# Optimization experiments

Measured on AMD Instinct MI355X. Metric: run time of the kernel, lower is better.

Reference implementation:

```python
import jax, jax.numpy as jnp
import numpy as np

N = 50000          # nodes
E = 800000         # directed edges (before self loops)
H = 2              # attention heads
NEG_SLOPE = 0.2    # PyG GATv2 default
EPS = 1e-5         # GraphNorm eps
DIMS = [(3, 64), (64, 64), (64, 64)]


def _gatv2_layer(x, Wl, Wr, att, b, src, dst):
    # x: [N, din]; Wl, Wr: [din, H*C]; att: [H, C]; b: [C]
    n = x.shape[0]
    h, c = att.shape
    xl = (x @ Wl).reshape(n, h, c)   # source-side transform
    xr = (x @ Wr).reshape(n, h, c)   # target-side transform
    # edge-wise GATv2 score: a . leaky_relu(xl[j] + xr[i])
    e = jax.nn.leaky_relu(xl[src] + xr[dst], NEG_SLOPE)      # [E, H, C]
    logit = jnp.einsum('ehc,hc->eh', e, att)                 # [E, H]
    # segment softmax over incoming edges of each target node
    m = jax.ops.segment_max(logit, dst, num_segments=n)      # [N, H]
    a = jnp.exp(logit - m[dst])
    z = jax.ops.segment_sum(a, dst, num_segments=n)
    alpha = a / z[dst]                                       # [E, H]
    out = jax.ops.segment_sum(alpha[:, :, None] * xl[src], dst, num_segments=n)  # [N, H, C]
    return out.mean(axis=1) + b                              # concat=False -> head mean


def _graph_norm(x, w, b, ms):
    # single-graph GraphNorm: x -> w * (x - ms*mean) / sqrt(var + eps) + b
    mu = x.mean(axis=0)
    o = x - ms * mu
    var = (o * o).mean(axis=0)
    return w * o * jax.lax.rsqrt(var + EPS) + b


def setup_inputs() -> dict:
    key = jax.random.key(0)
    ks = jax.random.split(key, 2 + 3 * len(DIMS))
    inp = {
        'x': jax.random.normal(ks[0], (N, 3), dtype=jnp.float32),
        'edge_index': jax.random.randint(ks[1], (2, E), 0, N, dtype=jnp.int32),
    }
    for i, (din, dout) in enumerate(DIMS, start=1):
        k0, k1, k2 = ks[2 + 3 * (i - 1):2 + 3 * i]
        s_in = np.float32(1.0 / np.sqrt(din))
        s_att = np.float32(1.0 / np.sqrt(dout))
        inp[f'Wl{i}'] = jax.random.normal(k0, (din, H * dout), dtype=jnp.float32) * s_in
        inp[f'Wr{i}'] = jax.random.normal(k1, (din, H * dout), dtype=jnp.float32) * s_in
        inp[f'att{i}'] = jax.random.normal(k2, (H, dout), dtype=jnp.float32) * s_att
        inp[f'b{i}'] = jnp.zeros((dout,), dtype=jnp.float32)
        inp[f'gw{i}'] = jnp.ones((dout,), dtype=jnp.float32)
        inp[f'gb{i}'] = jnp.zeros((dout,), dtype=jnp.float32)
        inp[f'gm{i}'] = jnp.ones((dout,), dtype=jnp.float32)
    return inp


def reference(x, edge_index,
              Wl1, Wr1, att1, b1, gw1, gb1, gm1,
              Wl2, Wr2, att2, b2, gw2, gb2, gm2,
              Wl3, Wr3, att3, b3, gw3, gb3, gm3):
    n = x.shape[0]
    loop = jnp.arange(n, dtype=edge_index.dtype)
    src = jnp.concatenate([edge_index[0], loop])  # add_self_loops=True
    dst = jnp.concatenate([edge_index[1], loop])
    layers = [(Wl1, Wr1, att1, b1, gw1, gb1, gm1),
              (Wl2, Wr2, att2, b2, gw2, gb2, gm2),
              (Wl3, Wr3, att3, b3, gw3, gb3, gm3)]
    for Wl, Wr, att, b, gw, gb, gm in layers:
        x = _gatv2_layer(x, Wl, Wr, att, b, src, dst)
        x = jax.nn.relu(_graph_norm(x, gw, gb, gm))
    return x
```

## Files before the change

### kernel.cpp

```cpp
#include <hip/hip_runtime.h>
#include <math.h>

#define NN 50000
#define NE 800000
#define TE (NE + NN)
#define HC 128
#define NEG_SLOPE 0.2f
#define EPSV 1e-5f
#define NBUCK 64
#define GGRID 782
#define WTB 128
#define ZB 52
#define ZERO_N4 18644

typedef __attribute__((ext_vector_type(8))) short bf16x8;
typedef __attribute__((ext_vector_type(4))) float f32x4;
union BfU { uint4 u; bf16x8 b; };

__device__ __forceinline__ unsigned short f2bf(float x) {
    unsigned u = __float_as_uint(x);
    unsigned r = (u + 0x7fff + ((u >> 16) & 1)) >> 16;
    return (unsigned short)r;
}


__global__ __launch_bounds__(256) void count_k(const int* __restrict__ dst,
                                               int* __restrict__ cnt,
                                               int* __restrict__ rank) {
    int e = blockIdx.x * 256 + threadIdx.x;
    if (e >= TE) return;
    int d = (e < NE) ? dst[e] : (e - NE);
    rank[e] = atomicAdd(&cnt[d], 1);
}

__global__ __launch_bounds__(1024) void scan1_k(const int* __restrict__ cnt,
                                                int* __restrict__ excl,
                                                int* __restrict__ aux) {
    __shared__ int wsum[16];
    int tid = threadIdx.x;
    int gid = blockIdx.x * 1024 + tid;
    int lane = tid & 63, wid = tid >> 6;
    int v = (gid < NN) ? cnt[gid] : 0;
    int x = v;
#pragma unroll
    for (int off = 1; off < 64; off <<= 1) {
        int t = __shfl_up(x, off, 64);
        if (lane >= off) x += t;
    }
    if (lane == 63) wsum[wid] = x;
    __syncthreads();
    if (wid == 0 && lane < 16) {
        int y = wsum[lane];
#pragma unroll
        for (int off = 1; off < 16; off <<= 1) {
            int t = __shfl_up(y, off, 64);
            if (lane >= off) y += t;
        }
        wsum[lane] = y;
    }
    __syncthreads();
    int base = (wid > 0) ? wsum[wid - 1] : 0;
    int incl = base + x;
    if (gid < NN) excl[gid] = incl - v;
    if (tid == 1023) aux[blockIdx.x] = incl;
}

__global__ __launch_bounds__(256) void scatter_k(const int* __restrict__ srcp,
                                                 const int* __restrict__ dstp,
                                                 const int* __restrict__ excl,
                                                 const int* __restrict__ aux,
                                                 const int* __restrict__ rank,
                                                 int* __restrict__ row_ptr,
                                                 int* __restrict__ col,
                                                 int nblk) {
    __shared__ int auxs[64];
    if (threadIdx.x < 64) {
        int lane = threadIdx.x;
        int v = (lane < nblk) ? aux[lane] : 0;
        int x = v;
#pragma unroll
        for (int off = 1; off < 64; off <<= 1) {
            int t = __shfl_up(x, off, 64);
            if (lane >= off) x += t;
        }
        auxs[lane] = x - v;
    }
    __syncthreads();
    int e = blockIdx.x * 256 + threadIdx.x;
    if (e >= TE) return;
    if (e <= NN) row_ptr[e] = (e == NN) ? TE : excl[e] + auxs[e >> 10];
    int s, d;
    if (e < NE) { s = srcp[e]; d = dstp[e]; } else { s = e - NE; d = s; }
    col[excl[d] + auxs[d >> 10] + rank[e]] = s << 8;
}

__device__ __forceinline__ void store_xlp(char* xlp, int row, int c0, const float* a) {
    unsigned hsel = (unsigned)c0 >> 6;
    unsigned dd = (unsigned)c0 & 31;
    unsigned sub = (c0 & 32) ? 2u : 0u;
    char* q = xlp + (size_t)row * 256 + hsel * 128 + 4 * dd + sub;
#pragma unroll
    for (int j = 0; j < 4; ++j)
        *(unsigned short*)(q + 4 * j) = f2bf(a[j]);
}


__global__ __launch_bounds__(256) void init_k(const float* __restrict__ x,
                                              const float* __restrict__ Wl1,
                                              const float* __restrict__ Wr1,
                                              char* __restrict__ xlp,
                                              float* __restrict__ xr,
                                              const float* __restrict__ Wl2,
                                              const float* __restrict__ Wr2,
                                              const float* __restrict__ Wl3,
                                              const float* __restrict__ Wr3,
                                              unsigned short* __restrict__ wt2,
                                              unsigned short* __restrict__ wt3,
                                              float4* __restrict__ zero4) {
    __shared__ float xs[32][72];
    __shared__ float ws[32][260];
    int b = blockIdx.x;
    int tid = threadIdx.x;

    if (b >= GGRID) {
        if (b < GGRID + WTB) {
            int idx = (b - GGRID) * 256 + tid;
            int l = idx >> 14;
            int rem = idx & 16383;
            int k = rem >> 8;
            int c = rem & 255;
            const float* W = (l == 0) ? (c < 128 ? Wl2 : Wr2) : (c < 128 ? Wl3 : Wr3);
            float v = W[k * 128 + (c & 127)];
            unsigned short* wt = (l == 0) ? wt2 : wt3;
            wt[c * 64 + k] = f2bf(v);
        } else {
            float4 zv; zv.x = zv.y = zv.z = zv.w = 0.f;
            for (int i = (b - GGRID - WTB) * 256 + tid; i < ZERO_N4; i += ZB * 256)
                zero4[i] = zv;
        }
        return;
    }

    int row0 = b * 64;
    int row_t = (tid >> 5) * 8;
    int c0 = (tid & 31) * 4;
    const int K = 3;

    float acc0[8][4];
    float acc1[8][4];
#pragma unroll
    for (int i = 0; i < 8; ++i)
#pragma unroll
        for (int j = 0; j < 4; ++j) { acc0[i][j] = 0.f; acc1[i][j] = 0.f; }

    for (int i = tid; i < 64 * K; i += 256) {
        int r = i / K;
        int k = i - r * K;
        int row = row0 + r;
        xs[k][r] = (row < NN) ? x[(size_t)row * K + k] : 0.f;
    }
    for (int i = tid; i < K * 64; i += 256) {
        int k = i >> 6;
        int cq = i & 63;
        const float* srcp = (cq < 32) ? &Wl1[(size_t)k * 128 + cq * 4]
                                      : &Wr1[(size_t)k * 128 + (cq - 32) * 4];
        float4 v = *(const float4*)srcp;
        *(float4*)&ws[k][cq * 4] = v;
    }
    __syncthreads();
    for (int k = 0; k < K; ++k) {
        float4 a0 = *(float4*)&xs[k][row_t];
        float4 a1 = *(float4*)&xs[k][row_t + 4];
        float4 b0 = *(float4*)&ws[k][c0];
        float4 b1 = *(float4*)&ws[k][c0 + 128];
        float av[8] = {a0.x, a0.y, a0.z, a0.w, a1.x, a1.y, a1.z, a1.w};
        float bl[4] = {b0.x, b0.y, b0.z, b0.w};
        float br[4] = {b1.x, b1.y, b1.z, b1.w};
#pragma unroll
        for (int i = 0; i < 8; ++i)
#pragma unroll
            for (int j = 0; j < 4; ++j) {
                acc0[i][j] += av[i] * bl[j];
                acc1[i][j] += av[i] * br[j];
            }
    }
#pragma unroll
    for (int i = 0; i < 8; ++i) {
        int row = row0 + row_t + i;
        if (row < NN) {
            store_xlp(xlp, row, c0, acc0[i]);
            float4 o1; o1.x = acc1[i][0]; o1.y = acc1[i][1]; o1.z = acc1[i][2]; o1.w = acc1[i][3];
            *(float4*)&xr[(size_t)row * HC + c0] = o1;
        }
    }
}

__device__ __forceinline__ void reduce_stats(const float* __restrict__ stats,
                                             const float* __restrict__ gw,
                                             const float* __restrict__ gb,
                                             const float* __restrict__ gm,
                                             float (*part)[128],
                                             float* __restrict__ cf_out) {
    int tid = threadIdx.x;
    int w = tid >> 6;
    int lane = tid & 63;
    float s = 0.f, s2 = 0.f;
    for (int b = 16 * w; b < 16 * w + 16; ++b) {
        s += stats[b * 128 + lane];
        s2 += stats[b * 128 + 64 + lane];
    }
    part[w][lane] = s;
    part[w][64 + lane] = s2;
    __syncthreads();
    if (tid < 64) {
        int c = tid;
        float sum = (part[0][c] + part[1][c]) + (part[2][c] + part[3][c]);
        float sum2 = (part[0][64 + c] + part[1][64 + c]) + (part[2][64 + c] + part[3][64 + c]);
        float inv_n = 1.f / (float)NN;
        float mu = sum * inv_n;
        float ex2 = sum2 * inv_n;
        float g = gm[c];
        float var = ex2 - 2.f * g * mu * mu + g * g * mu * mu;
        float rs = rsqrtf(var + EPSV);
        cf_out[c] = gw[c] * rs;
        cf_out[64 + c] = gb[c] - gw[c] * rs * g * mu;
    }
    __syncthreads();
}


__global__ __launch_bounds__(256) void gemm_mfma(const unsigned* __restrict__ hbf,
                                                 const float* __restrict__ stats,
                                                 const float* __restrict__ gw,
                                                 const float* __restrict__ gb,
                                                 const float* __restrict__ gm,
                                                 const unsigned short* __restrict__ wt,
                                                 char* __restrict__ xlp,
                                                 float* __restrict__ xr,
                                                 int n) {
    __shared__ unsigned short xs[64][72];
    __shared__ float part[4][128];
    __shared__ float cfS[128];
    int tid = threadIdx.x;
    int row0 = blockIdx.x * 64;

    reduce_stats(stats, gw, gb, gm, part, cfS);

    {
        int r = tid >> 2;
        int q = tid & 3;
        int row = row0 + r;
        unsigned pk[8];
        if (row < n) {
            const unsigned* hp = hbf + (size_t)row * 32 + (q & 1) * 16;
            uint4 u0 = *(const uint4*)(hp + 0);
            uint4 u1 = *(const uint4*)(hp + 4);
            uint4 u2 = *(const uint4*)(hp + 8);
            uint4 u3 = *(const uint4*)(hp + 12);
            unsigned hv[16] = {u0.x, u0.y, u0.z, u0.w, u1.x, u1.y, u1.z, u1.w,
                               u2.x, u2.y, u2.z, u2.w, u3.x, u3.y, u3.z, u3.w};
            bool hi = (q >> 1) != 0;
#pragma unroll
            for (int i = 0; i < 4; ++i) {
                float4 v;
                v.x = hi ? __uint_as_float(hv[4 * i + 0] & 0xffff0000u) : __uint_as_float(hv[4 * i + 0] << 16);
                v.y = hi ? __uint_as_float(hv[4 * i + 1] & 0xffff0000u) : __uint_as_float(hv[4 * i + 1] << 16);
                v.z = hi ? __uint_as_float(hv[4 * i + 2] & 0xffff0000u) : __uint_as_float(hv[4 * i + 2] << 16);
                v.w = hi ? __uint_as_float(hv[4 * i + 3] & 0xffff0000u) : __uint_as_float(hv[4 * i + 3] << 16);
                float4 cw = *(const float4*)&cfS[q * 16 + 4 * i];
                float4 cb = *(const float4*)&cfS[64 + q * 16 + 4 * i];
                float r0 = fmaxf(fmaf(cw.x, v.x, cb.x), 0.f);
                float r1 = fmaxf(fmaf(cw.y, v.y, cb.y), 0.f);
                float r2 = fmaxf(fmaf(cw.z, v.z, cb.z), 0.f);
                float r3 = fmaxf(fmaf(cw.w, v.w, cb.w), 0.f);
                pk[2 * i]     = (unsigned)f2bf(r0) | ((unsigned)f2bf(r1) << 16);
                pk[2 * i + 1] = (unsigned)f2bf(r2) | ((unsigned)f2bf(r3) << 16);
            }
        } else {
#pragma unroll
            for (int i = 0; i < 8; ++i) pk[i] = 0;
        }
        uint4* dst = (uint4*)&xs[r][q * 16];
        dst[0] = make_uint4(pk[0], pk[1], pk[2], pk[3]);
        dst[1] = make_uint4(pk[4], pk[5], pk[6], pk[7]);
    }
    __syncthreads();

    int w = tid >> 6;
    int lane = tid & 63;
    int m = lane & 15;
    int quad = lane >> 4;

    BfU a0, a1;
    a0.u = *(const uint4*)&xs[16 * w + m][quad * 8];
    a1.u = *(const uint4*)&xs[16 * w + m][32 + quad * 8];

    const char* wtb = (const char*)wt + (size_t)(m * 128 + quad * 16);

    f32x4 acc[16];
#pragma unroll
    for (int c = 0; c < 16; ++c) acc[c] = (f32x4){0.f, 0.f, 0.f, 0.f};
#pragma unroll
    for (int c = 0; c < 16; ++c) {
        BfU b0, b1;
        b0.u = *(const uint4*)(wtb + c * 2048);
        b1.u = *(const uint4*)(wtb + c * 2048 + 64);
        acc[c] = __builtin_amdgcn_mfma_f32_16x16x32_bf16(a0.b, b0.b, acc[c], 0, 0, 0);
        acc[c] = __builtin_amdgcn_mfma_f32_16x16x32_bf16(a1.b, b1.b, acc[c], 0, 0, 0);
    }

    int rbase = row0 + 16 * w + quad * 4;
#pragma unroll
    for (int c = 8; c < 16; ++c) {
        int colx = 16 * (c - 8) + m;
#pragma unroll
        for (int r = 0; r < 4; ++r) {
            int row = rbase + r;
            if (row < n) xr[(size_t)row * 128 + colx] = acc[c][r];
        }
    }
#pragma unroll
    for (int pi = 0; pi < 4; ++pi) {
        int c = (pi & 1) + (pi >> 1) * 4;
        int head = pi >> 1;
        int dd = (pi & 1) * 16 + m;
#pragma unroll
        for (int r = 0; r < 4; ++r) {
            int row = rbase + r;
            if (row < n) {
                unsigned val = (unsigned)f2bf(acc[c][r]) | ((unsigned)f2bf(acc[c + 2][r]) << 16);
                *(unsigned*)(xlp + (size_t)row * 256 + head * 128 + 4 * dd) = val;
            }
        }
    }
}


__global__ __launch_bounds__(256) void coef_k(const float* __restrict__ stats,
                                              const float* __restrict__ gw,
                                              const float* __restrict__ gb,
                                              const float* __restrict__ gm,
                                              float* __restrict__ cf) {
    __shared__ float part[4][128];
    reduce_stats(stats, gw, gb, gm, part, cf);
}


__device__ __forceinline__ void attn_batch(const char* __restrict__ xlp, int lp4,
                                           const int* offs, float2 xrv,
                                           float2 c1, float2 c2,
                                           bool b16, int my, int rem,
                                           float& zacc, float2& o) {
    unsigned pk[8];
#pragma unroll
    for (int j = 0; j < 8; ++j)
        pk[j] = *(const unsigned*)(xlp + (unsigned)(offs[j] + lp4));
    float2 l[8];
#pragma unroll
    for (int j = 0; j < 8; ++j) {
        l[j].x = __uint_as_float(pk[j] << 16);
        l[j].y = __uint_as_float(pk[j] & 0xffff0000u);
    }
    float u[8];
#pragma unroll
    for (int j = 0; j < 8; ++j) {
        float2 t; t.x = l[j].x + xrv.x; t.y = l[j].y + xrv.y;
        float2 q;
        q.x = fmaf(c1.x, t.x, c2.x * fabsf(t.x));
        q.y = fmaf(c1.y, t.y, c2.y * fabsf(t.y));
        u[j] = q.x + q.y;
    }
#pragma unroll
    for (int j = 0; j < 8; ++j) u[j] += __shfl_xor(u[j], 16, 64);
    float w0 = b16 ? u[0] : u[1];
    float w1 = b16 ? u[2] : u[3];
    float w2 = b16 ? u[4] : u[5];
    float w3 = b16 ? u[6] : u[7];
#pragma unroll
    for (int off = 8; off > 0; off >>= 1) {
        w0 += __shfl_xor(w0, off, 64);
        w1 += __shfl_xor(w1, off, 64);
        w2 += __shfl_xor(w2, off, 64);
        w3 += __shfl_xor(w3, off, 64);
    }
    float e0 = __expf(w0);
    float e1 = __expf(w1);
    float e2 = __expf(w2);
    float e3 = __expf(w3);
    if (rem < 8) {
        if (my >= rem)     e0 = 0.f;
        if (2 + my >= rem) e1 = 0.f;
        if (4 + my >= rem) e2 = 0.f;
        if (6 + my >= rem) e3 = 0.f;
    }
    zacc += (e0 + e1) + (e2 + e3);
    float s0 = __shfl_xor(e0, 16, 64);
    float s1 = __shfl_xor(e1, 16, 64);
    float s2 = __shfl_xor(e2, 16, 64);
    float s3 = __shfl_xor(e3, 16, 64);
    float p0 = b16 ? e0 : s0;
    float p1 = b16 ? s0 : e0;
    float p2 = b16 ? e1 : s1;
    float p3 = b16 ? s1 : e1;
    float p4 = b16 ? e2 : s2;
    float p5 = b16 ? s2 : e2;
    float p6 = b16 ? e3 : s3;
    float p7 = b16 ? s3 : e3;
    o.x = fmaf(p0, l[0].x, o.x); o.y = fmaf(p0, l[0].y, o.y);
    o.x = fmaf(p1, l[1].x, o.x); o.y = fmaf(p1, l[1].y, o.y);
    o.x = fmaf(p2, l[2].x, o.x); o.y = fmaf(p2, l[2].y, o.y);
    o.x = fmaf(p3, l[3].x, o.x); o.y = fmaf(p3, l[3].y, o.y);
    o.x = fmaf(p4, l[4].x, o.x); o.y = fmaf(p4, l[4].y, o.y);
    o.x = fmaf(p5, l[5].x, o.x); o.y = fmaf(p5, l[5].y, o.y);
    o.x = fmaf(p6, l[6].x, o.x); o.y = fmaf(p6, l[6].y, o.y);
    o.x = fmaf(p7, l[7].x, o.x); o.y = fmaf(p7, l[7].y, o.y);
}

__global__ __launch_bounds__(256) void attn_k(const char* __restrict__ xlp,
                                              const float* __restrict__ xr,
                                              const float* __restrict__ att,
                                              const float* __restrict__ bias,
                                              const int* __restrict__ row_ptr,
                                              const int* __restrict__ coloff,
                                              unsigned* __restrict__ hout,
                                              float* __restrict__ stats) {
    __shared__ float sb[4][64];
    int tid = threadIdx.x;
    int lane = tid & 63;
    int w = tid >> 6;
    int node = blockIdx.x * 4 + w;
    int laneh = lane & 31;
    int lanebase = ((lane >> 5) << 8) | (laneh << 2);
    bool b16 = (lane & 16) == 0;
    int my = b16 ? 0 : 1;
    int lp4 = lane * 4;

    const char* xrc = (const char*)xr;
    unsigned nodeoff = (unsigned)node << 9;

    float2 xrv;
    xrv.x = *(const float*)(xrc + nodeoff + lanebase);
    xrv.y = *(const float*)(xrc + nodeoff + lanebase + 128);
    float a1 = att[lanebase >> 2];
    float a2 = att[(lanebase >> 2) + 32];
    float2 c1; c1.x = 0.6f * a1; c1.y = 0.6f * a2;
    float2 c2; c2.x = 0.4f * a1; c2.y = 0.4f * a2;

    float zacc = 0.f;
    float2 o; o.x = 0.f; o.y = 0.f;

    int beg = __builtin_amdgcn_readfirstlane(row_ptr[node]);
    int end = __builtin_amdgcn_readfirstlane(row_ptr[node + 1]);

    int idx = beg;
    for (; idx + 8 <= end; idx += 8) {
        int offs[8];
#pragma unroll
        for (int j = 0; j < 8; ++j) offs[j] = coloff[idx + j];
        attn_batch(xlp, lp4, offs, xrv, c1, c2, b16, my, 8, zacc, o);
    }
    if (idx < end) {
        int rem = end - idx;
        int end1 = end - 1;
        int offs[8];
#pragma unroll
        for (int j = 0; j < 8; ++j) offs[j] = coloff[min(idx + j, end1)];
        attn_batch(xlp, lp4, offs, xrv, c1, c2, b16, my, rem, zacc, o);
    }
    float z = zacc + __shfl_xor(zacc, 16, 64);
    float zi = 1.0f / z;
    float2 t; t.x = o.x * zi; t.y = o.y * zi;
    float u1 = __shfl_xor(t.x, 32, 64);
    float u2 = __shfl_xor(t.y, 32, 64);
    if (lane < 32) {
        float r1 = fmaf(0.5f, t.x + u1, bias[laneh]);
        float r2 = fmaf(0.5f, t.y + u2, bias[laneh + 32]);
        hout[(size_t)node * 32 + laneh] = (unsigned)f2bf(r1) | ((unsigned)f2bf(r2) << 16);
        sb[w][laneh] = r1;
        sb[w][laneh + 32] = r2;
    }
    __syncthreads();
    if (tid < 64) {
        int c = tid;
        float v0 = sb[0][c], v1 = sb[1][c], v2 = sb[2][c], v3 = sb[3][c];
        float s = (v0 + v1) + (v2 + v3);
        float s2 = fmaf(v0, v0, v1 * v1) + fmaf(v2, v2, v3 * v3);
        float* bkt = stats + (size_t)(blockIdx.x & (NBUCK - 1)) * 128;
        atomicAdd(&bkt[c], s);
        atomicAdd(&bkt[64 + c], s2);
    }
}


__global__ __launch_bounds__(256) void apply_k(const unsigned* __restrict__ h,
                                               const float* __restrict__ cf,
                                               float* __restrict__ y) {
    int i = blockIdx.x * 256 + threadIdx.x;
    if (i >= NN * 8) return;
    int node = i >> 3;
    int j = (i & 7) * 4;
    uint4 u = *(const uint4*)(h + (size_t)node * 32 + j);
    float4 lo, hi;
    lo.x = __uint_as_float(u.x << 16); hi.x = __uint_as_float(u.x & 0xffff0000u);
    lo.y = __uint_as_float(u.y << 16); hi.y = __uint_as_float(u.y & 0xffff0000u);
    lo.z = __uint_as_float(u.z << 16); hi.z = __uint_as_float(u.z & 0xffff0000u);
    lo.w = __uint_as_float(u.w << 16); hi.w = __uint_as_float(u.w & 0xffff0000u);
    float4 cwl = *(const float4*)&cf[j];
    float4 cbl = *(const float4*)&cf[64 + j];
    float4 cwh = *(const float4*)&cf[32 + j];
    float4 cbh = *(const float4*)&cf[96 + j];
    float4 rl, rh;
    rl.x = fmaxf(fmaf(cwl.x, lo.x, cbl.x), 0.f);
    rl.y = fmaxf(fmaf(cwl.y, lo.y, cbl.y), 0.f);
    rl.z = fmaxf(fmaf(cwl.z, lo.z, cbl.z), 0.f);
    rl.w = fmaxf(fmaf(cwl.w, lo.w, cbl.w), 0.f);
    rh.x = fmaxf(fmaf(cwh.x, hi.x, cbh.x), 0.f);
    rh.y = fmaxf(fmaf(cwh.y, hi.y, cbh.y), 0.f);
    rh.z = fmaxf(fmaf(cwh.z, hi.z, cbh.z), 0.f);
    rh.w = fmaxf(fmaf(cwh.w, hi.w, cbh.w), 0.f);
    *(float4*)&y[(size_t)node * 64 + j] = rl;
    *(float4*)&y[(size_t)node * 64 + 32 + j] = rh;
}


extern "C" void kernel_launch(void* const* d_in, const int* in_sizes, int n_in,
                              void* d_out, int out_size, void* d_ws, size_t ws_size,
                              hipStream_t stream) {
    const float* x0 = (const float*)d_in[0];
    const int* ei = (const int*)d_in[1];
    const int* srcp = ei;
    const int* dstp = ei + NE;

    const float* Wl[3], *Wr[3], *att[3], *bv[3], *gw[3], *gb[3], *gm[3];
    for (int l = 0; l < 3; ++l) {
        int base = 2 + 7 * l;
        Wl[l] = (const float*)d_in[base + 0];
        Wr[l] = (const float*)d_in[base + 1];
        att[l] = (const float*)d_in[base + 2];
        bv[l] = (const float*)d_in[base + 3];
        gw[l] = (const float*)d_in[base + 4];
        gb[l] = (const float*)d_in[base + 5];
        gm[l] = (const float*)d_in[base + 6];
    }

    char* p = (char*)d_ws;
    auto take = [&](size_t bytes) -> void* {
        void* r = (void*)p;
        p += (bytes + 255) & ~(size_t)255;
        return r;
    };
    char* xlp = (char*)take((size_t)NN * 256);
    float* xr = (float*)take((size_t)NN * 128 * 4);
    unsigned* hb = (unsigned*)take((size_t)NN * 32 * 4);
    char* zr = (char*)take(298304);
    float* stats = (float*)zr;
    int* cnt = (int*)(zr + 98304);
    int* excl = (int*)take((size_t)NN * 4);
    int* row_ptr = (int*)take((size_t)(NN + 1) * 4);
    int* rank = (int*)take((size_t)TE * 4);
    int* col = (int*)take((size_t)TE * 4);
    int* aux = (int*)take(64 * 4);
    float* cf3 = (float*)take(128 * 4);
    unsigned short* wt2 = (unsigned short*)take(16384 * 2);
    unsigned short* wt3 = (unsigned short*)take(16384 * 2);

    int nblk = (NN + 1023) / 1024;
    int egrid = (TE + 255) / 256;

    init_k<<<GGRID + WTB + ZB, 256, 0, stream>>>(x0, Wl[0], Wr[0], xlp, xr,
                                                 Wl[1], Wr[1], Wl[2], Wr[2],
                                                 wt2, wt3, (float4*)zr);
    count_k<<<egrid, 256, 0, stream>>>(dstp, cnt, rank);
    scan1_k<<<nblk, 1024, 0, stream>>>(cnt, excl, aux);
    scatter_k<<<egrid, 256, 0, stream>>>(srcp, dstp, excl, aux, rank, row_ptr, col, nblk);

    int ggrid = (NN + 63) / 64;
    int agrid = NN / 4;
    for (int l = 0; l < 3; ++l) {
        if (l > 0)
            gemm_mfma<<<ggrid, 256, 0, stream>>>(hb, stats + (size_t)(l - 1) * NBUCK * 128,
                                                 gw[l - 1], gb[l - 1], gm[l - 1],
                                                 (l == 1) ? wt2 : wt3, xlp, xr, NN);
        attn_k<<<agrid, 256, 0, stream>>>(xlp, xr, att[l], bv[l], row_ptr, col, hb,
                                          stats + (size_t)l * NBUCK * 128);
    }
    coef_k<<<1, 256, 0, stream>>>(stats + (size_t)2 * NBUCK * 128, gw[2], gb[2], gm[2], cf3);
    apply_k<<<(NN * 8 + 255) / 256, 256, 0, stream>>>(hb, cf3, (float*)d_out);
}
```

Measured before the change: 363.1 us.

## Restructure attention to 16-lane edge groups with 16-byte gathers; fuse coef into apply

The attention kernel now splits each wavefront into four 16-lane groups. Each group handles two edges per iteration, and each lane loads 16 bytes (8 bf16 values) of the source feature row instead of 4 bytes. This cuts the number of shuffle reductions per edge and makes the gathers wider and fewer, at the cost of more registers per lane and a cross-group reduction at the end. Separately, the single-block coef kernel is removed and every apply block recomputes the GraphNorm coefficients itself. That saves one launch but repeats the stats reduction in every block.

Result: faster. 349.1 us (-3.8%).

```diff
diff --git a/kernel.cpp b/kernel.cpp
--- a/kernel.cpp
+++ b/kernel.cpp
@@ -336,84 +336,59 @@
 }
 
 
-__global__ __launch_bounds__(256) void coef_k(const float* __restrict__ stats,
-                                              const float* __restrict__ gw,
-                                              const float* __restrict__ gb,
-                                              const float* __restrict__ gm,
-                                              float* __restrict__ cf) {
-    __shared__ float part[4][128];
-    reduce_stats(stats, gw, gb, gm, part, cf);
-}
-
-
-__device__ __forceinline__ void attn_batch(const char* __restrict__ xlp, int lp4,
-                                           const int* offs, float2 xrv,
-                                           float2 c1, float2 c2,
-                                           bool b16, int my, int rem,
-                                           float& zacc, float2& o) {
-    unsigned pk[8];
-#pragma unroll
-    for (int j = 0; j < 8; ++j)
-        pk[j] = *(const unsigned*)(xlp + (unsigned)(offs[j] + lp4));
-    float2 l[8];
-#pragma unroll
-    for (int j = 0; j < 8; ++j) {
-        l[j].x = __uint_as_float(pk[j] << 16);
-        l[j].y = __uint_as_float(pk[j] & 0xffff0000u);
-    }
-    float u[8];
-#pragma unroll
-    for (int j = 0; j < 8; ++j) {
-        float2 t; t.x = l[j].x + xrv.x; t.y = l[j].y + xrv.y;
-        float2 q;
-        q.x = fmaf(c1.x, t.x, c2.x * fabsf(t.x));
-        q.y = fmaf(c1.y, t.y, c2.y * fabsf(t.y));
-        u[j] = q.x + q.y;
-    }
-#pragma unroll
-    for (int j = 0; j < 8; ++j) u[j] += __shfl_xor(u[j], 16, 64);
-    float w0 = b16 ? u[0] : u[1];
-    float w1 = b16 ? u[2] : u[3];
-    float w2 = b16 ? u[4] : u[5];
-    float w3 = b16 ? u[6] : u[7];
-#pragma unroll
-    for (int off = 8; off > 0; off >>= 1) {
-        w0 += __shfl_xor(w0, off, 64);
-        w1 += __shfl_xor(w1, off, 64);
-        w2 += __shfl_xor(w2, off, 64);
-        w3 += __shfl_xor(w3, off, 64);
-    }
+__device__ __forceinline__ void unpack8(uint4 q, float* l) {
+    l[0] = __uint_as_float(q.x << 16);
+    l[1] = __uint_as_float(q.x & 0xffff0000u);
+    l[2] = __uint_as_float(q.y << 16);
+    l[3] = __uint_as_float(q.y & 0xffff0000u);
+    l[4] = __uint_as_float(q.z << 16);
+    l[5] = __uint_as_float(q.z & 0xffff0000u);
+    l[6] = __uint_as_float(q.w << 16);
+    l[7] = __uint_as_float(q.w & 0xffff0000u);
+}
+
+__device__ __forceinline__ float logit_part(const float* l,
+                                            float4 xv0, float4 xv1,
+                                            float4 a0, float4 a1) {
+    float u1 = 0.f, u2 = 0.f, t;
+    t = l[0] + xv0.x; u1 = fmaf(a0.x, t, u1); u2 = fmaf(a0.x, fabsf(t), u2);
+    t = l[1] + xv1.x; u1 = fmaf(a1.x, t, u1); u2 = fmaf(a1.x, fabsf(t), u2);
+    t = l[2] + xv0.y; u1 = fmaf(a0.y, t, u1); u2 = fmaf(a0.y, fabsf(t), u2);
+    t = l[3] + xv1.y; u1 = fmaf(a1.y, t, u1); u2 = fmaf(a1.y, fabsf(t), u2);
+    t = l[4] + xv0.z; u1 = fmaf(a0.z, t, u1); u2 = fmaf(a0.z, fabsf(t), u2);
+    t = l[5] + xv1.z; u1 = fmaf(a1.z, t, u1); u2 = fmaf(a1.z, fabsf(t), u2);
+    t = l[6] + xv0.w; u1 = fmaf(a0.w, t, u1); u2 = fmaf(a0.w, fabsf(t), u2);
+    t = l[7] + xv1.w; u1 = fmaf(a1.w, t, u1); u2 = fmaf(a1.w, fabsf(t), u2);
+    return fmaf(0.6f, u1, 0.4f * u2);
+}
+
+__device__ __forceinline__ void attn_pair(const char* __restrict__ xlp, int lp16,
+                                          int off0, int off1, bool v0, bool v1,
+                                          float4 xv0, float4 xv1,
+                                          float4 a0, float4 a1,
+                                          float* o, float& zacc) {
+    uint4 q0 = *(const uint4*)(xlp + (unsigned)(off0 + lp16));
+    uint4 q1 = *(const uint4*)(xlp + (unsigned)(off1 + lp16));
+    float l0[8], l1[8];
+    unpack8(q0, l0);
+    unpack8(q1, l1);
+    float w0 = logit_part(l0, xv0, xv1, a0, a1);
+    float w1 = logit_part(l1, xv0, xv1, a0, a1);
+    w0 += __shfl_xor(w0, 1, 64);
+    w1 += __shfl_xor(w1, 1, 64);
+    w0 += __shfl_xor(w0, 2, 64);
+    w1 += __shfl_xor(w1, 2, 64);
+    w0 += __shfl_xor(w0, 4, 64);
+    w1 += __shfl_xor(w1, 4, 64);
     float e0 = __expf(w0);
     float e1 = __expf(w1);
-    float e2 = __expf(w2);
-    float e3 = __expf(w3);
-    if (rem < 8) {
-        if (my >= rem)     e0 = 0.f;
-        if (2 + my >= rem) e1 = 0.f;
-        if (4 + my >= rem) e2 = 0.f;
-        if (6 + my >= rem) e3 = 0.f;
-    }
-    zacc += (e0 + e1) + (e2 + e3);
-    float s0 = __shfl_xor(e0, 16, 64);
-    float s1 = __shfl_xor(e1, 16, 64);
-    float s2 = __shfl_xor(e2, 16, 64);
-    float s3 = __shfl_xor(e3, 16, 64);
-    float p0 = b16 ? e0 : s0;
-    float p1 = b16 ? s0 : e0;
-    float p2 = b16 ? e1 : s1;
-    float p3 = b16 ? s1 : e1;
-    float p4 = b16 ? e2 : s2;
-    float p5 = b16 ? s2 : e2;
-    float p6 = b16 ? e3 : s3;
-    float p7 = b16 ? s3 : e3;
-    o.x = fmaf(p0, l[0].x, o.x); o.y = fmaf(p0, l[0].y, o.y);
-    o.x = fmaf(p1, l[1].x, o.x); o.y = fmaf(p1, l[1].y, o.y);
-    o.x = fmaf(p2, l[2].x, o.x); o.y = fmaf(p2, l[2].y, o.y);
-    o.x = fmaf(p3, l[3].x, o.x); o.y = fmaf(p3, l[3].y, o.y);
-    o.x = fmaf(p4, l[4].x, o.x); o.y = fmaf(p4, l[4].y, o.y);
-    o.x = fmaf(p5, l[5].x, o.x); o.y = fmaf(p5, l[5].y, o.y);
-    o.x = fmaf(p6, l[6].x, o.x); o.y = fmaf(p6, l[6].y, o.y);
-    o.x = fmaf(p7, l[7].x, o.x); o.y = fmaf(p7, l[7].y, o.y);
+    if (!v0) e0 = 0.f;
+    if (!v1) e1 = 0.f;
+    zacc += e0 + e1;
+#pragma unroll
+    for (int k = 0; k < 8; ++k) o[k] = fmaf(e0, l0[k], o[k]);
+#pragma unroll
+    for (int k = 0; k < 8; ++k) o[k] = fmaf(e1, l1[k], o[k]);
 }
 
 __global__ __launch_bounds__(256) void attn_k(const char* __restrict__ xlp,
@@ -427,57 +402,67 @@
     __shared__ float sb[4][64];
     int tid = threadIdx.x;
     int lane = tid & 63;
-    int w = tid >> 6;
-    int node = blockIdx.x * 4 + w;
-    int laneh = lane & 31;
-    int lanebase = ((lane >> 5) << 8) | (laneh << 2);
-    bool b16 = (lane & 16) == 0;
-    int my = b16 ? 0 : 1;
-    int lp4 = lane * 4;
-
-    const char* xrc = (const char*)xr;
-    unsigned nodeoff = (unsigned)node << 9;
-
-    float2 xrv;
-    xrv.x = *(const float*)(xrc + nodeoff + lanebase);
-    xrv.y = *(const float*)(xrc + nodeoff + lanebase + 128);
-    float a1 = att[lanebase >> 2];
-    float a2 = att[(lanebase >> 2) + 32];
-    float2 c1; c1.x = 0.6f * a1; c1.y = 0.6f * a2;
-    float2 c2; c2.x = 0.4f * a1; c2.y = 0.4f * a2;
-
+    int wv = tid >> 6;
+    int node = blockIdx.x * 4 + wv;
+    int t16 = lane & 15;
+    int slot = (lane >> 4) * 2;
+    int head = t16 >> 3;
+    int dd = (t16 & 7) * 4;
+    int lp16 = t16 * 16;
+    int cbase = head * 64 + dd;
+
+    const float* xrow = xr + (size_t)node * 128;
+    float4 xv0 = *(const float4*)(xrow + cbase);
+    float4 xv1 = *(const float4*)(xrow + cbase + 32);
+    float4 a0 = *(const float4*)(att + cbase);
+    float4 a1 = *(const float4*)(att + cbase + 32);
+
+    float o[8];
+#pragma unroll
+    for (int k = 0; k < 8; ++k) o[k] = 0.f;
     float zacc = 0.f;
-    float2 o; o.x = 0.f; o.y = 0.f;
 
     int beg = __builtin_amdgcn_readfirstlane(row_ptr[node]);
     int end = __builtin_amdgcn_readfirstlane(row_ptr[node + 1]);
 
     int idx = beg;
     for (; idx + 8 <= end; idx += 8) {
-        int offs[8];
-#pragma unroll
-        for (int j = 0; j < 8; ++j) offs[j] = coloff[idx + j];
-        attn_batch(xlp, lp4, offs, xrv, c1, c2, b16, my, 8, zacc, o);
+        int off0 = coloff[idx + slot];
+        int off1 = coloff[idx + slot + 1];
+        attn_pair(xlp, lp16, off0, off1, true, true, xv0, xv1, a0, a1, o, zacc);
     }
     if (idx < end) {
-        int rem = end - idx;
-        int end1 = end - 1;
-        int offs[8];
-#pragma unroll
-        for (int j = 0; j < 8; ++j) offs[j] = coloff[min(idx + j, end1)];
-        attn_batch(xlp, lp4, offs, xrv, c1, c2, b16, my, rem, zacc, o);
-    }
+        int e1 = end - 1;
+        int i0 = idx + slot, i1 = idx + slot + 1;
+        int off0 = coloff[min(i0, e1)];
+        int off1 = coloff[min(i1, e1)];
+        attn_pair(xlp, lp16, off0, off1, i0 < end, i1 < end, xv0, xv1, a0, a1, o, zacc);
+    }
+
     float z = zacc + __shfl_xor(zacc, 16, 64);
+    z += __shfl_xor(z, 32, 64);
     float zi = 1.0f / z;
-    float2 t; t.x = o.x * zi; t.y = o.y * zi;
-    float u1 = __shfl_xor(t.x, 32, 64);
-    float u2 = __shfl_xor(t.y, 32, 64);
-    if (lane < 32) {
-        float r1 = fmaf(0.5f, t.x + u1, bias[laneh]);
-        float r2 = fmaf(0.5f, t.y + u2, bias[laneh + 32]);
-        hout[(size_t)node * 32 + laneh] = (unsigned)f2bf(r1) | ((unsigned)f2bf(r2) << 16);
-        sb[w][laneh] = r1;
-        sb[w][laneh + 32] = r2;
+    float r[8];
+#pragma unroll
+    for (int k = 0; k < 8; ++k) {
+        float v = o[k] + __shfl_xor(o[k], 16, 64);
+        v += __shfl_xor(v, 32, 64);
+        v *= zi;
+        float p = __shfl_xor(v, 8, 64);
+        r[k] = 0.5f * (v + p);
+    }
+    if (lane < 8) {
+        float4 b0 = *(const float4*)(bias + dd);
+        float4 b1 = *(const float4*)(bias + dd + 32);
+        float rl0 = r[0] + b0.x, rl1 = r[2] + b0.y, rl2 = r[4] + b0.z, rl3 = r[6] + b0.w;
+        float rh0 = r[1] + b1.x, rh1 = r[3] + b1.y, rh2 = r[5] + b1.z, rh3 = r[7] + b1.w;
+        unsigned pk0 = (unsigned)f2bf(rl0) | ((unsigned)f2bf(rh0) << 16);
+        unsigned pk1 = (unsigned)f2bf(rl1) | ((unsigned)f2bf(rh1) << 16);
+        unsigned pk2 = (unsigned)f2bf(rl2) | ((unsigned)f2bf(rh2) << 16);
+        unsigned pk3 = (unsigned)f2bf(rl3) | ((unsigned)f2bf(rh3) << 16);
+        *(uint4*)&hout[(size_t)node * 32 + dd] = make_uint4(pk0, pk1, pk2, pk3);
+        *(float4*)&sb[wv][dd] = make_float4(rl0, rl1, rl2, rl3);
+        *(float4*)&sb[wv][dd + 32] = make_float4(rh0, rh1, rh2, rh3);
     }
     __syncthreads();
     if (tid < 64) {
@@ -493,8 +478,15 @@
 
 
 __global__ __launch_bounds__(256) void apply_k(const unsigned* __restrict__ h,
-                                               const float* __restrict__ cf,
+                                               const float* __restrict__ stats,
+                                               const float* __restrict__ gw,
+                                               const float* __restrict__ gb,
+                                               const float* __restrict__ gm,
                                                float* __restrict__ y) {
+    __shared__ float part[4][128];
+    __shared__ float cfS[128];
+    reduce_stats(stats, gw, gb, gm, part, cfS);
+
     int i = blockIdx.x * 256 + threadIdx.x;
     if (i >= NN * 8) return;
     int node = i >> 3;
@@ -505,10 +497,10 @@
     lo.y = __uint_as_float(u.y << 16); hi.y = __uint_as_float(u.y & 0xffff0000u);
     lo.z = __uint_as_float(u.z << 16); hi.z = __uint_as_float(u.z & 0xffff0000u);
     lo.w = __uint_as_float(u.w << 16); hi.w = __uint_as_float(u.w & 0xffff0000u);
-    float4 cwl = *(const float4*)&cf[j];
-    float4 cbl = *(const float4*)&cf[64 + j];
-    float4 cwh = *(const float4*)&cf[32 + j];
-    float4 cbh = *(const float4*)&cf[96 + j];
+    float4 cwl = *(const float4*)&cfS[j];
+    float4 cbl = *(const float4*)&cfS[64 + j];
+    float4 cwh = *(const float4*)&cfS[32 + j];
+    float4 cbh = *(const float4*)&cfS[96 + j];
     float4 rl, rh;
     rl.x = fmaxf(fmaf(cwl.x, lo.x, cbl.x), 0.f);
     rl.y = fmaxf(fmaf(cwl.y, lo.y, cbl.y), 0.f);
@@ -560,7 +552,6 @@
     int* rank = (int*)take((size_t)TE * 4);
     int* col = (int*)take((size_t)TE * 4);
     int* aux = (int*)take(64 * 4);
-    float* cf3 = (float*)take(128 * 4);
     unsigned short* wt2 = (unsigned short*)take(16384 * 2);
     unsigned short* wt3 = (unsigned short*)take(16384 * 2);
 
@@ -584,6 +575,6 @@
         attn_k<<<agrid, 256, 0, stream>>>(xlp, xr, att[l], bv[l], row_ptr, col, hb,
                                           stats + (size_t)l * NBUCK * 128);
     }
-    coef_k<<<1, 256, 0, stream>>>(stats + (size_t)2 * NBUCK * 128, gw[2], gb[2], gm[2], cf3);
-    apply_k<<<(NN * 8 + 255) / 256, 256, 0, stream>>>(hb, cf3, (float*)d_out);
-}
+    apply_k<<<(NN * 8 + 255) / 256, 256, 0, stream>>>(hb, stats + (size_t)2 * NBUCK * 128,
+                                                      gw[2], gb[2], gm[2], (float*)d_out);
+}
```
